# Kernel optimization log

Hardware: AMD Instinct MI355X
Metric: run time of the kernel (lower is better)

## Reference

```python
import math
import jax, jax.numpy as jnp
import numpy as np

SM_K = 5

def make_sm_kernel(kernel_size=SM_K, sigma_e=1.2, sigma_i=1.4):
    center = kernel_size // 2
    xx, yy = jnp.meshgrid(jnp.arange(kernel_size, dtype=jnp.float32),
                          jnp.arange(kernel_size, dtype=jnp.float32), indexing='ij')
    xx = xx - center
    yy = yy - center
    g_e = jnp.exp(-(xx ** 2 + yy ** 2) / (2.0 * sigma_e ** 2))
    g_i = jnp.exp(-(xx ** 2 + yy ** 2) / (2.0 * sigma_i ** 2))
    dog = g_e / (2.0 * math.pi * sigma_e ** 2) - g_i / (2.0 * math.pi * sigma_i ** 2)
    return dog / dog[center, center]  # (5,5), normalized so center == 1


def setup_inputs() -> dict:
    key = jax.random.key(0)
    k1, k2 = jax.random.split(key)
    B, Cin, H, W = 16, 64, 128, 128
    Cout, K = 64, 5
    x = jax.random.normal(k1, (B, Cin, H, W), dtype=jnp.float32)
    weight_range = 25.0 / math.sqrt(Cin * K * K)
    weight = weight_range * jnp.abs(jax.random.normal(k2, (Cout, Cin, K, K), dtype=jnp.float32))
    return {"x": x, "weight": weight}


def reference(x, weight):
    PAD = 2
    dn = ('NCHW', 'OIHW', 'NCHW')
    Cout = weight.shape[0]
    K = weight.shape[-1]

    # symmetric_pad -> F.pad reflect
    xp = jnp.pad(x, ((0, 0), (0, 0), (PAD, PAD), (PAD, PAD)), mode='reflect')

    # w = weight.abs(); F.normalize(w, p=2, dim=1): L2 norm over in_channels per (o, kh, kw)
    w = jnp.abs(weight)
    nrm = jnp.sqrt(jnp.sum(w * w, axis=1, keepdims=True))
    w_n = w / jnp.maximum(nrm, 1e-12)

    # cosine similarity: conv with normalized weights / input patch norm
    conv = jax.lax.conv_general_dilated(xp, w_n, (1, 1), 'VALID', dimension_numbers=dn)
    # conv(x^2, ones_like(w)) yields identical values for every output channel;
    # compute once with a single-output-channel ones kernel and broadcast.
    ones_k = jnp.ones((1, x.shape[1], K, K), dtype=x.dtype)
    xsq_sum = jax.lax.conv_general_dilated(xp * xp, ones_k, (1, 1), 'VALID', dimension_numbers=dn)
    y = conv / jnp.sqrt(xsq_sum + 1e-8)  # (B, Cout, H, W)

    # surround modulation: depthwise conv with fixed 5x5 DoG kernel, padding 2
    sm = make_sm_kernel()
    sm_k = jnp.broadcast_to(sm[None, None].astype(y.dtype), (Cout, 1, SM_K, SM_K))
    y = jax.lax.conv_general_dilated(y, sm_k, (1, 1), [(SM_K // 2, SM_K // 2)] * 2,
                                     dimension_numbers=dn, feature_group_count=Cout)
    return y
```

## Files before the change

### kernel.cpp

```cpp
#include <hip/hip_runtime.h>
#include <hip/hip_bf16.h>
#include <math.h>

#define B_   16
#define CIN  64
#define COUT 64
#define H_   128
#define W_   128
#define KK   25
#define HW   (H_ * W_)
#define XT_PLANE ((size_t)B_ * HW * 32)

typedef short  bf16x8 __attribute__((ext_vector_type(8)));
typedef short  s16x4  __attribute__((ext_vector_type(4)));
typedef float  f32x16 __attribute__((ext_vector_type(16)));
typedef float  f32x4  __attribute__((ext_vector_type(4)));
typedef float  f32x2  __attribute__((ext_vector_type(2)));

__device__ __forceinline__ short f2bs(float v) {
    __hip_bfloat16 h = __float2bfloat16(v);
    return *reinterpret_cast<short*>(&h);
}
__device__ __forceinline__ float bs2f(short s) {
    unsigned int u = ((unsigned int)(unsigned short)s) << 16;
    return __uint_as_float(u);
}

__global__ __launch_bounds__(256) void k_wprep(const float* __restrict__ w,
                                               short* __restrict__ wnb2) {
    __shared__ float wl[CIN * KK];
    __shared__ float inv[KK];
    const int o   = blockIdx.x;
    const int tid = threadIdx.x;

    for (int idx = tid; idx < CIN * KK; idx += 256)
        wl[idx] = w[(size_t)o * (CIN * KK) + idx];
    __syncthreads();
    if (tid < KK) {
        float s = 0.f;
        #pragma unroll 8
        for (int i = 0; i < CIN; ++i) { float v = wl[i * KK + tid]; s += v * v; }
        inv[tid] = 1.f / fmaxf(sqrtf(s), 1e-12f);
    }
    __syncthreads();
    const int tt = o >> 5, n = o & 31;
    for (int idx = tid; idx < CIN * KK; idx += 256) {
        int ci = idx & 63, kk = idx >> 6;
        int ks = ci >> 4, q = (ci >> 3) & 1, j = ci & 7;
        int l = q * 32 + n;
        wnb2[((size_t)((kk * 4 + ks) * 2 + tt) * 64 + l) * 8 + j] =
            f2bs(fabsf(wl[ci * KK + kk]) * inv[kk]);
    }
}

__global__ __launch_bounds__(256) void k_xprep(const float* __restrict__ x,
                                               short* __restrict__ xt,
                                               float* __restrict__ xsqg) {
    __shared__ float tile[64][65];
    __shared__ float ps[4][64];
    const int b = blockIdx.z, h = blockIdx.y, w0 = blockIdx.x * 64;
    const int tid = threadIdx.x;

    const float* xb = x + (size_t)b * CIN * HW + h * W_ + w0;
    {
        int wl = tid & 63, c0 = tid >> 6;
        float sq = 0.f;
        #pragma unroll
        for (int cc = 0; cc < 16; ++cc) {
            float v = xb[(size_t)(c0 * 16 + cc) * HW + wl];
            tile[c0 * 16 + cc][wl] = v;
            sq += v * v;
        }
        ps[c0][wl] = sq;
    }
    __syncthreads();

    const size_t pixbase = (size_t)b * HW + h * W_ + w0;
    if (tid < 64)
        xsqg[pixbase + tid] = ps[0][tid] + ps[1][tid] + ps[2][tid] + ps[3][tid];

    {
        int c8 = tid & 7;
        int half = c8 >> 2, sl = c8 & 3;
        short* dp = xt + (size_t)half * XT_PLANE;
        #pragma unroll
        for (int rep = 0; rep < 2; ++rep) {
            int p = (tid >> 3) + rep * 32;
            bf16x8 v;
            #pragma unroll
            for (int j = 0; j < 8; ++j) v[j] = f2bs(tile[c8 * 8 + j][p]);
            *(bf16x8*)&dp[(pixbase + p) * 32 + sl * 8] = v;
        }
    }
}

#define XP 40
#define NR 12
#define NC 36
#define NS (NR * NC)
#define TP 264

__global__ __launch_bounds__(256, 4) void k_conv(const short* __restrict__ xt,
                                                 const float* __restrict__ xsqg,
                                                 const short* __restrict__ wnb2,
                                                 __hip_bfloat16* __restrict__ t) {
    __shared__ short xin[NS * XP];
    __shared__ float s2win[NS];
    __shared__ int   soff[NS];
    __shared__ float xsq[256];

    const int tid  = threadIdx.x;
    const int lane = tid & 63;
    const int wv   = tid >> 6;
    const int n    = lane & 31;
    const int q    = lane >> 5;
    const int b    = blockIdx.z;
    const int h0   = blockIdx.y * 8;
    const int w0   = blockIdx.x * 32;

    const size_t pixbase = (size_t)b * HW;

    for (int s = tid; s < NS; s += 256) {
        int r = s / NC, c = s - r * NC;
        int hh = h0 - 2 + r; hh = hh < 0 ? -hh : (hh > H_ - 1 ? 2 * (H_ - 1) - hh : hh);
        int ww = w0 - 2 + c; ww = ww < 0 ? -ww : (ww > W_ - 1 ? 2 * (W_ - 1) - ww : ww);
        int off = hh * W_ + ww;
        soff[s] = off;
        s2win[s] = xsqg[pixbase + off];
    }
    __syncthreads();

    {
        int hr = tid >> 5, cl = tid & 31;
        float a = 0.f;
        #pragma unroll
        for (int kh = 0; kh < 5; ++kh)
            #pragma unroll
            for (int kw = 0; kw < 5; ++kw)
                a += s2win[(hr + kh) * NC + cl + kw];
        xsq[tid] = a;
    }

    const short* wb = wnb2 + (size_t)lane * 8;

    f32x16 acc00, acc01, acc10, acc11;
    #pragma unroll
    for (int i = 0; i < 16; ++i) { acc00[i] = 0.f; acc01[i] = 0.f; acc10[i] = 0.f; acc11[i] = 0.f; }

    #pragma unroll
    for (int half = 0; half < 2; ++half) {
        const short* xph = xt + (size_t)half * XT_PLANE + pixbase * 32;
        for (int i = tid; i < NS * 4; i += 256) {
            int s = i >> 2, c8 = i & 3;
            *(bf16x8*)&xin[s * XP + c8 * 8] =
                *(const bf16x8*)&xph[(size_t)soff[s] * 32 + c8 * 8];
        }
        __syncthreads();

        #pragma unroll 5
        for (int kk = 0; kk < KK; ++kk) {
            const int kh = kk / 5, kw = kk % 5;
            const int sp0 = (2 * wv + kh) * NC + n + kw;
            #pragma unroll
            for (int ks2 = 0; ks2 < 2; ++ks2) {
                const int ks = half * 2 + ks2;
                const int ko = ks2 * 16 + q * 8;
                bf16x8 a0 = *(const bf16x8*)&xin[sp0 * XP + ko];
                bf16x8 a1 = *(const bf16x8*)&xin[(sp0 + NC) * XP + ko];
                bf16x8 b0 = *(const bf16x8*)&wb[(size_t)((kk * 4 + ks) * 2 + 0) * 512];
                bf16x8 b1 = *(const bf16x8*)&wb[(size_t)((kk * 4 + ks) * 2 + 1) * 512];
                acc00 = __builtin_amdgcn_mfma_f32_32x32x16_bf16(a0, b0, acc00, 0, 0, 0);
                acc01 = __builtin_amdgcn_mfma_f32_32x32x16_bf16(a0, b1, acc01, 0, 0, 0);
                acc10 = __builtin_amdgcn_mfma_f32_32x32x16_bf16(a1, b0, acc10, 0, 0, 0);
                acc11 = __builtin_amdgcn_mfma_f32_32x32x16_bf16(a1, b1, acc11, 0, 0, 0);
            }
        }
        __syncthreads();
    }

    short* trans = xin;
    const int hrA = 2 * wv, hrB = 2 * wv + 1;
    #pragma unroll
    for (int g4 = 0; g4 < 4; ++g4) {
        int wc0 = 8 * g4 + 4 * q;
        s16x4 v00, v01, v10, v11;
        #pragma unroll
        for (int j = 0; j < 4; ++j) {
            float ia = rsqrtf(xsq[hrA * 32 + wc0 + j] + 1e-8f);
            float ib = rsqrtf(xsq[hrB * 32 + wc0 + j] + 1e-8f);
            v00[j] = f2bs(acc00[4 * g4 + j] * ia);
            v01[j] = f2bs(acc01[4 * g4 + j] * ia);
            v10[j] = f2bs(acc10[4 * g4 + j] * ib);
            v11[j] = f2bs(acc11[4 * g4 + j] * ib);
        }
        *(s16x4*)&trans[n * TP        + hrA * 32 + wc0] = v00;
        *(s16x4*)&trans[(32 + n) * TP + hrA * 32 + wc0] = v01;
        *(s16x4*)&trans[n * TP        + hrB * 32 + wc0] = v10;
        *(s16x4*)&trans[(32 + n) * TP + hrB * 32 + wc0] = v11;
    }
    __syncthreads();

    #pragma unroll
    for (int u = tid; u < 512; u += 256) {
        int oc = u >> 3, hr = u & 7;
        const short* src = &trans[oc * TP + hr * 32];
        __hip_bfloat16* dst = t + ((size_t)(b * COUT + oc) * H_ + h0 + hr) * W_ + w0;
        float4 a0 = *(const float4*)(src);
        float4 a1 = *(const float4*)(src + 8);
        float4 a2 = *(const float4*)(src + 16);
        float4 a3 = *(const float4*)(src + 24);
        *(float4*)(dst)      = a0;
        *(float4*)(dst + 8)  = a1;
        *(float4*)(dst + 16) = a2;
        *(float4*)(dst + 24) = a3;
    }
}

__global__ __launch_bounds__(256) void k_dog(const __hip_bfloat16* __restrict__ t,
                                             float* __restrict__ out) {
    __shared__ float tile[36 * 136];
    __shared__ float sm_s[25];
    const int bo  = blockIdx.y;
    const int h0  = blockIdx.x * 32;
    const int tid = threadIdx.x;

    if (tid < 25) {
        const float se2 = 2.f * 1.2f * 1.2f;
        const float si2 = 2.f * 1.4f * 1.4f;
        const float twopi = 6.28318530717958647692f;
        const float ae = 1.f / (twopi * 1.2f * 1.2f);
        const float ai = 1.f / (twopi * 1.4f * 1.4f);
        const float c0 = ae - ai;
        int dx = tid / 5 - 2, dy = tid % 5 - 2;
        float r2 = (float)(dx * dx + dy * dy);
        sm_s[tid] = (ae * expf(-r2 / se2) - ai * expf(-r2 / si2)) / c0;
    }

    const __hip_bfloat16* tc = t + (size_t)bo * HW;
    for (int idx = tid; idx < 36 * 16; idx += 256) {
        int rr = idx >> 4, g = idx & 15;
        int hh = h0 - 2 + rr;
        float v[8];
        if (hh >= 0 && hh < H_) {
            bf16x8 a = *(const bf16x8*)&tc[hh * W_ + g * 8];
            #pragma unroll
            for (int j = 0; j < 8; ++j) v[j] = bs2f(a[j]);
        } else {
            #pragma unroll
            for (int j = 0; j < 8; ++j) v[j] = 0.f;
        }
        float* dst = &tile[rr * 136 + 2 + g * 8];
        *(f32x2*)(dst)     = (f32x2){v[0], v[1]};
        *(f32x4*)(dst + 2) = (f32x4){v[2], v[3], v[4], v[5]};
        *(f32x2*)(dst + 6) = (f32x2){v[6], v[7]};
    }
    if (tid < 36 * 4) {
        int rr = tid >> 2, c = tid & 3;
        tile[rr * 136 + (c < 2 ? c : 128 + c)] = 0.f;
    }
    __syncthreads();

    float smr[25];
    #pragma unroll
    for (int kk = 0; kk < 25; ++kk) smr[kk] = sm_s[kk];

    const int cq = tid & 31;
    const int r0 = tid >> 5;
    #pragma unroll
    for (int rr = 0; rr < 4; ++rr) {
        int r = r0 + 8 * rr;
        float s0 = 0.f, s1 = 0.f, s2 = 0.f, s3 = 0.f;
        #pragma unroll
        for (int kh = 0; kh < 5; ++kh) {
            const float* row = &tile[(r + kh) * 136 + cq * 4];
            f32x4 v0 = *(const f32x4*)(row);
            f32x4 v1 = *(const f32x4*)(row + 4);
            float vv[8] = { v0[0], v0[1], v0[2], v0[3], v1[0], v1[1], v1[2], v1[3] };
            #pragma unroll
            for (int kw = 0; kw < 5; ++kw) {
                float cf = smr[kh * 5 + kw];
                s0 += cf * vv[kw];
                s1 += cf * vv[kw + 1];
                s2 += cf * vv[kw + 2];
                s3 += cf * vv[kw + 3];
            }
        }
        float4 o4 = make_float4(s0, s1, s2, s3);
        *(float4*)&out[((size_t)bo * H_ + h0 + r) * W_ + cq * 4] = o4;
    }
}

extern "C" void kernel_launch(void* const* d_in, const int* in_sizes, int n_in,
                              void* d_out, int out_size, void* d_ws, size_t ws_size,
                              hipStream_t stream) {
    const float* x = (const float*)d_in[0];
    const float* w = (const float*)d_in[1];

    __hip_bfloat16* t = (__hip_bfloat16*)d_ws;

    short* xt    = (short*)d_out;
    float* xsqg  = (float*)((char*)d_out + 33554432);
    short* wnb2  = (short*)((char*)d_out + (size_t)67108864 - 204800);

    k_wprep<<<COUT, 256, 0, stream>>>(w, wnb2);

    dim3 gx(W_ / 64, H_, B_);
    k_xprep<<<gx, 256, 0, stream>>>(x, xt, xsqg);

    dim3 g2(W_ / 32, H_ / 8, B_);
    k_conv<<<g2, 256, 0, stream>>>(xt, xsqg, wnb2, t);

    dim3 g3(H_ / 32, B_ * COUT);
    k_dog<<<g3, 256, 0, stream>>>(t, (float*)d_out);
}
```

Baseline: 190.5 us.

## Merge prep kernels, stage weights in double-buffered LDS, swizzle input tile

The weight and input preparation kernels are merged into one launch, with an extra grid slice handling the weight normalization. In the conv kernel, weights are now prefetched into registers and staged per kernel tap into a double-buffered LDS region, so they are no longer read straight from global memory on each MFMA. The input tile drops its padded row stride in favour of an XOR swizzle to avoid bank conflicts. This adds a __syncthreads per tap and removes unrolling of the tap loop, which could reduce overlap between loads and MFMAs.

```diff
diff --git a/kernel.cpp b/kernel.cpp
--- a/kernel.cpp
+++ b/kernel.cpp
@@ -26,40 +26,43 @@
     return __uint_as_float(u);
 }
 
-__global__ __launch_bounds__(256) void k_wprep(const float* __restrict__ w,
-                                               short* __restrict__ wnb2) {
-    __shared__ float wl[CIN * KK];
-    __shared__ float inv[KK];
-    const int o   = blockIdx.x;
+__global__ __launch_bounds__(256) void k_prep(const float* __restrict__ x,
+                                              const float* __restrict__ w,
+                                              short* __restrict__ xt,
+                                              float* __restrict__ xsqg,
+                                              short* __restrict__ wnb2) {
     const int tid = threadIdx.x;
 
-    for (int idx = tid; idx < CIN * KK; idx += 256)
-        wl[idx] = w[(size_t)o * (CIN * KK) + idx];
-    __syncthreads();
-    if (tid < KK) {
-        float s = 0.f;
-        #pragma unroll 8
-        for (int i = 0; i < CIN; ++i) { float v = wl[i * KK + tid]; s += v * v; }
-        inv[tid] = 1.f / fmaxf(sqrtf(s), 1e-12f);
-    }
-    __syncthreads();
-    const int tt = o >> 5, n = o & 31;
-    for (int idx = tid; idx < CIN * KK; idx += 256) {
-        int ci = idx & 63, kk = idx >> 6;
-        int ks = ci >> 4, q = (ci >> 3) & 1, j = ci & 7;
-        int l = q * 32 + n;
-        wnb2[((size_t)((kk * 4 + ks) * 2 + tt) * 64 + l) * 8 + j] =
-            f2bs(fabsf(wl[ci * KK + kk]) * inv[kk]);
-    }
-}
-
-__global__ __launch_bounds__(256) void k_xprep(const float* __restrict__ x,
-                                               short* __restrict__ xt,
-                                               float* __restrict__ xsqg) {
+    if (blockIdx.z == B_) {
+        if (blockIdx.x != 0 || blockIdx.y >= COUT) return;
+        __shared__ float wl[CIN * KK];
+        __shared__ float inv[KK];
+        const int o = blockIdx.y;
+
+        for (int idx = tid; idx < CIN * KK; idx += 256)
+            wl[idx] = w[(size_t)o * (CIN * KK) + idx];
+        __syncthreads();
+        if (tid < KK) {
+            float s = 0.f;
+            #pragma unroll 8
+            for (int i = 0; i < CIN; ++i) { float v = wl[i * KK + tid]; s += v * v; }
+            inv[tid] = 1.f / fmaxf(sqrtf(s), 1e-12f);
+        }
+        __syncthreads();
+        const int tt = o >> 5, n = o & 31;
+        for (int idx = tid; idx < CIN * KK; idx += 256) {
+            int ci = idx & 63, kk = idx >> 6;
+            int ks = ci >> 4, q = (ci >> 3) & 1, j = ci & 7;
+            int l = q * 32 + n;
+            wnb2[((size_t)((kk * 4 + ks) * 2 + tt) * 64 + l) * 8 + j] =
+                f2bs(fabsf(wl[ci * KK + kk]) * inv[kk]);
+        }
+        return;
+    }
+
     __shared__ float tile[64][65];
     __shared__ float ps[4][64];
     const int b = blockIdx.z, h = blockIdx.y, w0 = blockIdx.x * 64;
-    const int tid = threadIdx.x;
 
     const float* xb = x + (size_t)b * CIN * HW + h * W_ + w0;
     {
@@ -94,7 +97,6 @@
     }
 }
 
-#define XP 40
 #define NR 12
 #define NC 36
 #define NS (NR * NC)
@@ -104,10 +106,12 @@
                                                  const float* __restrict__ xsqg,
                                                  const short* __restrict__ wnb2,
                                                  __hip_bfloat16* __restrict__ t) {
-    __shared__ short xin[NS * XP];
-    __shared__ float s2win[NS];
-    __shared__ int   soff[NS];
-    __shared__ float xsq[256];
+    __shared__ __align__(16) short pool[20160];
+    short* xin   = pool;
+    short* bbuf  = pool + 13824;
+    float* s2win = (float*)&pool[17920];
+    int*   soff  = (int*)&pool[18784];
+    float* xsq   = (float*)&pool[19648];
 
     const int tid  = threadIdx.x;
     const int lane = tid & 63;
@@ -141,34 +145,36 @@
         xsq[tid] = a;
     }
 
-    const short* wb = wnb2 + (size_t)lane * 8;
-
     f32x16 acc00, acc01, acc10, acc11;
     #pragma unroll
     for (int i = 0; i < 16; ++i) { acc00[i] = 0.f; acc01[i] = 0.f; acc10[i] = 0.f; acc11[i] = 0.f; }
 
-    #pragma unroll
     for (int half = 0; half < 2; ++half) {
         const short* xph = xt + (size_t)half * XT_PLANE + pixbase * 32;
         for (int i = tid; i < NS * 4; i += 256) {
             int s = i >> 2, c8 = i & 3;
-            *(bf16x8*)&xin[s * XP + c8 * 8] =
+            *(bf16x8*)&xin[s * 32 + ((c8 ^ (s & 3)) << 3)] =
                 *(const bf16x8*)&xph[(size_t)soff[s] * 32 + c8 * 8];
         }
+        const short* wsrc = wnb2 + half * 2048 + (size_t)tid * 8;
+        bf16x8 breg = *(const bf16x8*)&wsrc[0];
         __syncthreads();
 
-        #pragma unroll 5
         for (int kk = 0; kk < KK; ++kk) {
+            *(bf16x8*)&bbuf[(kk & 1) * 2048 + tid * 8] = breg;
+            __syncthreads();
+            if (kk < KK - 1) breg = *(const bf16x8*)&wsrc[(kk + 1) * 4096];
             const int kh = kk / 5, kw = kk % 5;
             const int sp0 = (2 * wv + kh) * NC + n + kw;
+            const int sx = sp0 & 3;
+            const short* bb = &bbuf[(kk & 1) * 2048];
             #pragma unroll
             for (int ks2 = 0; ks2 < 2; ++ks2) {
-                const int ks = half * 2 + ks2;
-                const int ko = ks2 * 16 + q * 8;
-                bf16x8 a0 = *(const bf16x8*)&xin[sp0 * XP + ko];
-                bf16x8 a1 = *(const bf16x8*)&xin[(sp0 + NC) * XP + ko];
-                bf16x8 b0 = *(const bf16x8*)&wb[(size_t)((kk * 4 + ks) * 2 + 0) * 512];
-                bf16x8 b1 = *(const bf16x8*)&wb[(size_t)((kk * 4 + ks) * 2 + 1) * 512];
+                const int cA = ((ks2 * 2 + q) ^ sx) << 3;
+                bf16x8 a0 = *(const bf16x8*)&xin[sp0 * 32 + cA];
+                bf16x8 a1 = *(const bf16x8*)&xin[(sp0 + NC) * 32 + cA];
+                bf16x8 b0 = *(const bf16x8*)&bb[(ks2 * 2 + 0) * 512 + lane * 8];
+                bf16x8 b1 = *(const bf16x8*)&bb[(ks2 * 2 + 1) * 512 + lane * 8];
                 acc00 = __builtin_amdgcn_mfma_f32_32x32x16_bf16(a0, b0, acc00, 0, 0, 0);
                 acc01 = __builtin_amdgcn_mfma_f32_32x32x16_bf16(a0, b1, acc01, 0, 0, 0);
                 acc10 = __builtin_amdgcn_mfma_f32_32x32x16_bf16(a1, b0, acc10, 0, 0, 0);
@@ -178,7 +184,7 @@
         __syncthreads();
     }
 
-    short* trans = xin;
+    short* trans = pool;
     const int hrA = 2 * wv, hrB = 2 * wv + 1;
     #pragma unroll
     for (int g4 = 0; g4 < 4; ++g4) {
@@ -302,10 +308,8 @@
     float* xsqg  = (float*)((char*)d_out + 33554432);
     short* wnb2  = (short*)((char*)d_out + (size_t)67108864 - 204800);
 
-    k_wprep<<<COUT, 256, 0, stream>>>(w, wnb2);
-
-    dim3 gx(W_ / 64, H_, B_);
-    k_xprep<<<gx, 256, 0, stream>>>(x, xt, xsqg);
+    dim3 gx(W_ / 64, H_, B_ + 1);
+    k_prep<<<gx, 256, 0, stream>>>(x, w, xt, xsqg, wnb2);
 
     dim3 g2(W_ / 32, H_ / 8, B_);
     k_conv<<<g2, 256, 0, stream>>>(xt, xsqg, wnb2, t);
```

Result: slower. 201.1 us (+5.6%).
